# Kernel optimization log

Measured on AMD Instinct MI355X. Metric: run time of the kernel, lower is better.

Reference implementation:

```python
import jax, jax.numpy as jnp
import numpy as np

B, C, H, W = 16, 512, 32, 32
HID = 4 * C


def setup_inputs() -> dict:
    key = jax.random.key(0)
    k_x, k_w1, k_w2 = jax.random.split(key, 3)
    x = jax.random.normal(k_x, (B, C, H, W), dtype=jnp.float32)
    # 1x1 conv weights stored as [out, in] matrices (kernel_size=1)
    w1 = jax.random.normal(k_w1, (HID, C), dtype=jnp.float32) * (1.0 / np.sqrt(C))
    b1 = jnp.zeros((HID,), dtype=jnp.float32)
    w2 = jax.random.normal(k_w2, (C, HID), dtype=jnp.float32) * (1.0 / np.sqrt(HID))
    b2 = jnp.zeros((C,), dtype=jnp.float32)
    return {"x": x, "w1": w1, "b1": b1, "w2": w2, "b2": b2}


def reference(x, w1, b1, w2, b2):
    Bd, Cd, Hd, Wd = x.shape
    scale = Cd ** (-0.5)
    xf = x.reshape(Bd, Cd, Hd * Wd)          # [B, C, N]
    q = jnp.swapaxes(xf, -1, -2)              # [B, N, C]
    # full spatial self-attention: scores [B, N, N]
    attn = jax.nn.softmax(jnp.einsum('bnc,bcm->bnm', q, xf) * scale, axis=-1)
    out = jnp.einsum('bnm,bmc->bnc', attn, q)  # [B, N, C]
    # 1x1-conv FFN applied per spatial position
    h = jax.nn.relu(jnp.einsum('bnc,dc->bnd', out, w1) + b1)   # [B, N, 4C]
    y = jnp.einsum('bnd,cd->bnc', h, w2) + b2                  # [B, N, C]
    y = jnp.swapaxes(y, -1, -2).reshape(Bd, Cd, Hd, Wd)
    return y + x
```

## Files before the change

kernel.cpp:

```cpp
#include <hip/hip_runtime.h>

#define BATCH 16
#define CH    512
#define NSP   1024
#define HIDD  2048

typedef __bf16 bf16x8 __attribute__((ext_vector_type(8)));
typedef float floatx4 __attribute__((ext_vector_type(4)));

__device__ __forceinline__ float bf2f(unsigned short u) {
    union { unsigned int i; float f; } v; v.i = ((unsigned int)u) << 16; return v.f;
}
__device__ __forceinline__ unsigned short f2bf(float f) {
    union { float f; unsigned int i; } v; v.f = f;
    unsigned int i = v.i;
    return (unsigned short)((i + 0x7FFFu + ((i >> 16) & 1u)) >> 16);
}

__device__ __forceinline__ void gload16(const void* g, void* l) {
    __builtin_amdgcn_global_load_lds(
        (__attribute__((address_space(1))) unsigned int*)(g),
        (__attribute__((address_space(3))) unsigned int*)(l),
        16, 0, 0);
}

template<int EPI, int MAP>
__global__ __launch_bounds__(256, 4)
void gemm_bt(const unsigned short* __restrict__ A,
             const unsigned short* __restrict__ Bm,
             void* __restrict__ Cout,
             int Nn, int K,
             long sAb, long sBb, long sCb,
             const float* __restrict__ bias, float scale,
             const float* __restrict__ resid)
{
    __shared__ unsigned short sA[2][128 * 32];
    __shared__ unsigned short sB[2][128 * 32];

    const int tid  = threadIdx.x;
    const int lane = tid & 63;
    const int w    = tid >> 6;
    const int quad = lane >> 4;
    const int l15  = lane & 15;
    const int mw   = (w >> 1) * 64;
    const int nw   = (w & 1) * 64;

    const int F = blockIdx.x;
    int m0, n0, b;
    if constexpr (MAP == 0) {
        const int xcd = F & 7, s = F >> 3;
        b = xcd + ((s >> 6) << 3);
        const int j = s & 63; m0 = (j >> 3) << 7; n0 = (j & 7) << 7;
    } else if constexpr (MAP == 1) {
        const int xcd = F & 7, s = F >> 3;
        b = xcd + ((s >> 5) << 3);
        const int j = s & 31; m0 = (j >> 2) << 7; n0 = (j & 3) << 7;
    } else if constexpr (MAP == 2) {
        const int xcd = F & 7, s = F >> 3;
        b = 0; m0 = ((xcd << 4) + (s >> 4)) << 7; n0 = (s & 15) << 7;
    } else {
        const int xcd = F & 7, s = F >> 3;
        b = 0; m0 = (s & 3) << 7; n0 = ((xcd << 4) + (s >> 2)) << 7;
    }

    A  += (size_t)b * sAb;
    Bm += (size_t)b * sBb;

    const int srow = lane >> 2;
    const int sg   = (lane & 3) ^ ((lane >> 3) & 3);
    const unsigned short* pA = A  + (size_t)(m0 + w * 32 + srow) * K + sg * 8;
    const unsigned short* pB = Bm + (size_t)(n0 + w * 32 + srow) * K + sg * 8;
    const size_t rowskip16 = (size_t)16 * K;
    const int woff = w * 1024;

    floatx4 acc[4][4];
#pragma unroll
    for (int i = 0; i < 4; i++)
#pragma unroll
        for (int j = 0; j < 4; j++) acc[i][j] = (floatx4){0.f, 0.f, 0.f, 0.f};

    const int rslot = ((l15 >> 1) & 3);

    const int nIter = K >> 5;

    {
        unsigned short* dA = &sA[0][0] + woff;
        unsigned short* dB = &sB[0][0] + woff;
        gload16(pA,             dA);
        gload16(pA + rowskip16, dA + 512);
        gload16(pB,             dB);
        gload16(pB + rowskip16, dB + 512);
    }

    for (int it = 0; it < nIter; ++it) {
        __syncthreads();

        if (it + 1 < nIter) {
            const int koff = (it + 1) << 5;
            unsigned short* dA = &sA[(it + 1) & 1][0] + woff;
            unsigned short* dB = &sB[(it + 1) & 1][0] + woff;
            gload16(pA + koff,             dA);
            gload16(pA + koff + rowskip16, dA + 512);
            gload16(pB + koff,             dB);
            gload16(pB + koff + rowskip16, dB + 512);
        }

        const unsigned short* bufA = &sA[it & 1][0];
        const unsigned short* bufB = &sB[it & 1][0];
        bf16x8 af[4], bfr[4];
#pragma unroll
        for (int mi = 0; mi < 4; mi++)
            af[mi] = *(const bf16x8*)(bufA + (mw + mi * 16 + l15) * 32
                                      + (quad ^ rslot) * 8);
#pragma unroll
        for (int ni = 0; ni < 4; ni++)
            bfr[ni] = *(const bf16x8*)(bufB + (nw + ni * 16 + l15) * 32
                                       + (quad ^ rslot) * 8);
#pragma unroll
        for (int mi = 0; mi < 4; mi++)
#pragma unroll
            for (int ni = 0; ni < 4; ni++)
                acc[mi][ni] = __builtin_amdgcn_mfma_f32_16x16x32_bf16(
                    af[mi], bfr[ni], acc[mi][ni], 0, 0, 0);
    }

    if constexpr (EPI == 4) {
        float* Of = (float*)Cout;
#pragma unroll
        for (int ni = 0; ni < 4; ni++) {
            const int j  = n0 + nw + ni * 16 + l15;
            const int bb = j >> 10, ns = j & 1023;
            const size_t cbase = (size_t)bb * CH * NSP + ns;
#pragma unroll
            for (int mi = 0; mi < 4; mi++) {
                const int ibase = m0 + mw + mi * 16 + quad * 4;
#pragma unroll
                for (int r = 0; r < 4; r++) {
                    const int c = ibase + r;
                    const size_t a = cbase + (size_t)c * NSP;
                    Of[a] = acc[mi][ni][r] + bias[c] + resid[a];
                }
            }
        }
    } else {
        unsigned short* Cb = (unsigned short*)Cout + (size_t)b * sCb;
#pragma unroll
        for (int ni = 0; ni < 4; ni++) {
            const int n = n0 + nw + ni * 16 + l15;
            float bv = 0.f;
            if constexpr (EPI == 2) bv = bias[n];
#pragma unroll
            for (int mi = 0; mi < 4; mi++) {
                const int mbase = m0 + mw + mi * 16 + quad * 4;
#pragma unroll
                for (int r = 0; r < 4; r++) {
                    float v = acc[mi][ni][r];
                    if constexpr (EPI == 0) v *= scale;
                    if constexpr (EPI == 2) v = fmaxf(v + bv, 0.f);
                    Cb[(size_t)(mbase + r) * Nn + n] = f2bf(v);
                }
            }
        }
    }
}

__global__ __launch_bounds__(256)
void pack_x_kernel(const float* __restrict__ x,
                   unsigned short* __restrict__ Xbf,
                   unsigned short* __restrict__ XT)
{
    __shared__ float tile[32][33];
    const int tx = threadIdx.x, ty = threadIdx.y;
    const int n0 = blockIdx.x * 32, c0 = blockIdx.y * 32, b = blockIdx.z;
    const size_t base = (size_t)b * CH * NSP;
#pragma unroll
    for (int i = ty; i < 32; i += 8) {
        float v = x[base + (size_t)(c0 + i) * NSP + n0 + tx];
        tile[i][tx] = v;
        Xbf[base + (size_t)(c0 + i) * NSP + n0 + tx] = f2bf(v);
    }
    __syncthreads();
    const size_t tbase = (size_t)b * NSP * CH;
#pragma unroll
    for (int i = ty; i < 32; i += 8)
        XT[tbase + (size_t)(n0 + i) * CH + c0 + tx] = f2bf(tile[tx][i]);
}

__global__ __launch_bounds__(256)
void cast_bf16_kernel(const float* __restrict__ src,
                      unsigned short* __restrict__ dst, int n)
{
    int i = blockIdx.x * 256 + threadIdx.x;
    if (i < n) dst[i] = f2bf(src[i]);
}

__global__ __launch_bounds__(256)
void softmax_kernel(unsigned short* __restrict__ S)
{
    const int row = blockIdx.x;
    unsigned short* p = S + (size_t)row * NSP;
    const int t = threadIdx.x;

    ushort4 u = ((const ushort4*)p)[t];
    float v0 = bf2f(u.x), v1 = bf2f(u.y), v2 = bf2f(u.z), v3 = bf2f(u.w);

    float m = fmaxf(fmaxf(v0, v1), fmaxf(v2, v3));
#pragma unroll
    for (int off = 32; off > 0; off >>= 1) m = fmaxf(m, __shfl_xor(m, off));
    __shared__ float redmax[4], redsum[4];
    const int wid = t >> 6;
    if ((t & 63) == 0) redmax[wid] = m;
    __syncthreads();
    m = fmaxf(fmaxf(redmax[0], redmax[1]), fmaxf(redmax[2], redmax[3]));

    v0 = __expf(v0 - m); v1 = __expf(v1 - m);
    v2 = __expf(v2 - m); v3 = __expf(v3 - m);
    float s = v0 + v1 + v2 + v3;
#pragma unroll
    for (int off = 32; off > 0; off >>= 1) s += __shfl_xor(s, off);
    if ((t & 63) == 0) redsum[wid] = s;
    __syncthreads();
    s = redsum[0] + redsum[1] + redsum[2] + redsum[3];

    const float inv = 1.0f / s;
    ushort4 o;
    o.x = f2bf(v0 * inv); o.y = f2bf(v1 * inv);
    o.z = f2bf(v2 * inv); o.w = f2bf(v3 * inv);
    ((ushort4*)p)[t] = o;
}

extern "C" void kernel_launch(void* const* d_in, const int* in_sizes, int n_in,
                              void* d_out, int out_size, void* d_ws, size_t ws_size,
                              hipStream_t stream)
{
    const float* x  = (const float*)d_in[0];
    const float* w1 = (const float*)d_in[1];
    const float* b1 = (const float*)d_in[2];
    const float* w2 = (const float*)d_in[3];
    const float* b2 = (const float*)d_in[4];
    float* out = (float*)d_out;

    char* ws = (char*)d_ws;
    unsigned short* Xbf = (unsigned short*)ws; ws += (size_t)BATCH * CH * NSP * 2;
    unsigned short* XT  = (unsigned short*)ws; ws += (size_t)BATCH * NSP * CH * 2;
    unsigned short* W1b = (unsigned short*)ws; ws += (size_t)HIDD * CH * 2;
    unsigned short* W2b = (unsigned short*)ws; ws += (size_t)CH * HIDD * 2;
    unsigned short* P   = (unsigned short*)ws; ws += (size_t)BATCH * NSP * NSP * 2;
    unsigned short* O   = (unsigned short*)ws; ws += (size_t)BATCH * NSP * CH * 2;
    unsigned short* Hb  = (unsigned short*)ws; ws += (size_t)BATCH * NSP * HIDD * 2;

    const dim3 blk(256);

    pack_x_kernel<<<dim3(NSP / 32, CH / 32, BATCH), dim3(32, 8), 0, stream>>>(x, Xbf, XT);
    cast_bf16_kernel<<<dim3((HIDD * CH) / 256), blk, 0, stream>>>(w1, W1b, HIDD * CH);
    cast_bf16_kernel<<<dim3((CH * HIDD) / 256), blk, 0, stream>>>(w2, W2b, CH * HIDD);

    gemm_bt<0, 0><<<dim3(1024), blk, 0, stream>>>(
        XT, XT, P, NSP, CH,
        (long)NSP * CH, (long)NSP * CH, (long)NSP * NSP, nullptr,
        0.04419417382415922f, nullptr);

    softmax_kernel<<<dim3(BATCH * NSP), blk, 0, stream>>>(P);

    gemm_bt<1, 1><<<dim3(512), blk, 0, stream>>>(
        P, Xbf, O, CH, NSP,
        (long)NSP * NSP, (long)CH * NSP, (long)NSP * CH, nullptr, 1.f, nullptr);

    gemm_bt<2, 2><<<dim3(2048), blk, 0, stream>>>(
        O, W1b, Hb, HIDD, CH, 0, 0, 0, b1, 1.f, nullptr);

    gemm_bt<4, 3><<<dim3(512), blk, 0, stream>>>(
        W2b, Hb, out, BATCH * NSP, HIDD, 0, 0, 0, b2, 1.f, x);
}
```

Measured before the change: 282.2 us.

## Load B fragments directly to registers and triple-buffer A in LDS

The GEMM main loop stops staging the B operand through shared memory. Each wave now loads its B MFMA fragments straight from global memory into a pair of ping-pong registers, prefetched one step ahead. The A operand moves to a three-slot LDS ring with two-deep prefetch, and the explicit vmcnt wait plus barrier replaces __syncthreads. The aim is to cut LDS traffic and barrier stalls, at the cost of more VGPRs (occupancy hint lowered from 4 to 3) and uncoalesced direct global reads of B. The MAP==2 block mapping also drops its XCD-aware swizzle in favour of a plain linear order.

```diff
diff --git a/kernel.cpp b/kernel.cpp
--- a/kernel.cpp
+++ b/kernel.cpp
@@ -23,9 +23,10 @@
         (__attribute__((address_space(3))) unsigned int*)(l),
         16, 0, 0);
 }
+#define MEMFENCE asm volatile("" ::: "memory")
 
 template<int EPI, int MAP>
-__global__ __launch_bounds__(256, 4)
+__global__ __launch_bounds__(256, 3)
 void gemm_bt(const unsigned short* __restrict__ A,
              const unsigned short* __restrict__ Bm,
              void* __restrict__ Cout,
@@ -34,8 +35,7 @@
              const float* __restrict__ bias, float scale,
              const float* __restrict__ resid)
 {
-    __shared__ unsigned short sA[2][128 * 32];
-    __shared__ unsigned short sB[2][128 * 32];
+    __shared__ unsigned short sA[3][128 * 32];
 
     const int tid  = threadIdx.x;
     const int lane = tid & 63;
@@ -56,8 +56,7 @@
         b = xcd + ((s >> 5) << 3);
         const int j = s & 31; m0 = (j >> 2) << 7; n0 = (j & 3) << 7;
     } else if constexpr (MAP == 2) {
-        const int xcd = F & 7, s = F >> 3;
-        b = 0; m0 = ((xcd << 4) + (s >> 4)) << 7; n0 = (s & 15) << 7;
+        b = 0; m0 = (F >> 4) << 7; n0 = (F & 15) << 7;
     } else {
         const int xcd = F & 7, s = F >> 3;
         b = 0; m0 = (s & 3) << 7; n0 = ((xcd << 4) + (s >> 2)) << 7;
@@ -68,10 +67,13 @@
 
     const int srow = lane >> 2;
     const int sg   = (lane & 3) ^ ((lane >> 3) & 3);
-    const unsigned short* pA = A  + (size_t)(m0 + w * 32 + srow) * K + sg * 8;
-    const unsigned short* pB = Bm + (size_t)(n0 + w * 32 + srow) * K + sg * 8;
+    const unsigned short* pA = A + (size_t)(m0 + w * 32 + srow) * K + sg * 8;
     const size_t rowskip16 = (size_t)16 * K;
     const int woff = w * 1024;
+    const int rslot = ((l15 >> 1) & 3);
+
+    const unsigned short* pBf = Bm + (size_t)(n0 + nw + l15) * K + quad * 8;
+    const size_t bstride = (size_t)16 * K;
 
     floatx4 acc[4][4];
 #pragma unroll
@@ -79,49 +81,58 @@
 #pragma unroll
         for (int j = 0; j < 4; j++) acc[i][j] = (floatx4){0.f, 0.f, 0.f, 0.f};
 
-    const int rslot = ((l15 >> 1) & 3);
-
     const int nIter = K >> 5;
+    const int kLast = K - 32;
+
+    bf16x8 bP[4], bQ[4];
 
     {
-        unsigned short* dA = &sA[0][0] + woff;
-        unsigned short* dB = &sB[0][0] + woff;
-        gload16(pA,             dA);
-        gload16(pA + rowskip16, dA + 512);
-        gload16(pB,             dB);
-        gload16(pB + rowskip16, dB + 512);
-    }
-
-    for (int it = 0; it < nIter; ++it) {
-        __syncthreads();
-
-        if (it + 1 < nIter) {
-            const int koff = (it + 1) << 5;
-            unsigned short* dA = &sA[(it + 1) & 1][0] + woff;
-            unsigned short* dB = &sB[(it + 1) & 1][0] + woff;
-            gload16(pA + koff,             dA);
-            gload16(pA + koff + rowskip16, dA + 512);
-            gload16(pB + koff,             dB);
-            gload16(pB + koff + rowskip16, dB + 512);
-        }
-
-        const unsigned short* bufA = &sA[it & 1][0];
-        const unsigned short* bufB = &sB[it & 1][0];
-        bf16x8 af[4], bfr[4];
+        unsigned short* d0 = &sA[0][0] + woff;
+        unsigned short* d1 = &sA[1][0] + woff;
+        gload16(pA,                 d0);
+        gload16(pA + rowskip16,     d0 + 512);
+        gload16(pA + 32,            d1);
+        gload16(pA + 32 + rowskip16, d1 + 512);
+        MEMFENCE;
+#pragma unroll
+        for (int ni = 0; ni < 4; ni++)
+            bP[ni] = *(const bf16x8*)(pBf + ni * bstride);
+        MEMFENCE;
+    }
+
+    auto body = [&](int it, bf16x8* bcur, bf16x8* bnext) {
+        asm volatile("s_waitcnt vmcnt(6)\n\ts_barrier" ::: "memory");
+
+        int r = it; while (r >= 3) r -= 3;
+        int rs = r + 2; if (rs >= 3) rs -= 3;
+        const int kst = (it + 2) * 32 <= kLast ? (it + 2) * 32 : kLast;
+        unsigned short* dS = &sA[0][0] + rs * 4096 + woff;
+        gload16(pA + kst,             dS);
+        gload16(pA + kst + rowskip16, dS + 512);
+        MEMFENCE;
+        const int kb = (it + 1) * 32 <= kLast ? (it + 1) * 32 : kLast;
+#pragma unroll
+        for (int ni = 0; ni < 4; ni++)
+            bnext[ni] = *(const bf16x8*)(pBf + ni * bstride + kb);
+        MEMFENCE;
+
+        const unsigned short* bufR = &sA[0][0] + r * 4096;
+        bf16x8 af[4];
 #pragma unroll
         for (int mi = 0; mi < 4; mi++)
-            af[mi] = *(const bf16x8*)(bufA + (mw + mi * 16 + l15) * 32
+            af[mi] = *(const bf16x8*)(bufR + (mw + mi * 16 + l15) * 32
                                       + (quad ^ rslot) * 8);
-#pragma unroll
-        for (int ni = 0; ni < 4; ni++)
-            bfr[ni] = *(const bf16x8*)(bufB + (nw + ni * 16 + l15) * 32
-                                       + (quad ^ rslot) * 8);
 #pragma unroll
         for (int mi = 0; mi < 4; mi++)
 #pragma unroll
             for (int ni = 0; ni < 4; ni++)
                 acc[mi][ni] = __builtin_amdgcn_mfma_f32_16x16x32_bf16(
-                    af[mi], bfr[ni], acc[mi][ni], 0, 0, 0);
+                    af[mi], bcur[ni], acc[mi][ni], 0, 0, 0);
+    };
+
+    for (int it = 0; it < nIter; it += 2) {
+        body(it,     bP, bQ);
+        body(it + 1, bQ, bP);
     }
 
     if constexpr (EPI == 4) {
@@ -135,10 +146,10 @@
             for (int mi = 0; mi < 4; mi++) {
                 const int ibase = m0 + mw + mi * 16 + quad * 4;
 #pragma unroll
-                for (int r = 0; r < 4; r++) {
-                    const int c = ibase + r;
+                for (int r2 = 0; r2 < 4; r2++) {
+                    const int c = ibase + r2;
                     const size_t a = cbase + (size_t)c * NSP;
-                    Of[a] = acc[mi][ni][r] + bias[c] + resid[a];
+                    Of[a] = acc[mi][ni][r2] + bias[c] + resid[a];
                 }
             }
         }
@@ -153,11 +164,11 @@
             for (int mi = 0; mi < 4; mi++) {
                 const int mbase = m0 + mw + mi * 16 + quad * 4;
 #pragma unroll
-                for (int r = 0; r < 4; r++) {
-                    float v = acc[mi][ni][r];
+                for (int r2 = 0; r2 < 4; r2++) {
+                    float v = acc[mi][ni][r2];
                     if constexpr (EPI == 0) v *= scale;
                     if constexpr (EPI == 2) v = fmaxf(v + bv, 0.f);
-                    Cb[(size_t)(mbase + r) * Nn + n] = f2bf(v);
+                    Cb[(size_t)(mbase + r2) * Nn + n] = f2bf(v);
                 }
             }
         }
```

Measured after the change: 360.7 us. +27.8%, slower.

## Triple-buffer LDS tiles with two-stage prefetch and partial vmcnt waits

Applied to the files above, without the earlier changes.

Moves the GEMM mainloop from double to triple buffering in shared memory. Two K-tiles are now prefetched ahead, and each iteration waits only for the oldest outstanding global-to-LDS loads (vmcnt(4)) before the barrier instead of a full sync, so more load latency can overlap with MFMA work. On the last iterations the prefetch is clamped to reissue the final tile rather than branching. Launch bounds drop to 3 blocks per CU to make room for the larger LDS footprint, and the MAP==2 block-to-tile mapping drops its XCD swizzle in favour of a plain linear order, which may change L2 locality. Possible risks are an LDS race, since the buffer written by each prefetch was read in the previous iteration and is protected only by the next barrier, and lower occupancy.

```diff
diff --git a/kernel.cpp b/kernel.cpp
--- a/kernel.cpp
+++ b/kernel.cpp
@@ -23,9 +23,10 @@
         (__attribute__((address_space(3))) unsigned int*)(l),
         16, 0, 0);
 }
+#define MEMFENCE asm volatile("" ::: "memory")
 
 template<int EPI, int MAP>
-__global__ __launch_bounds__(256, 4)
+__global__ __launch_bounds__(256, 3)
 void gemm_bt(const unsigned short* __restrict__ A,
              const unsigned short* __restrict__ Bm,
              void* __restrict__ Cout,
@@ -34,8 +35,8 @@
              const float* __restrict__ bias, float scale,
              const float* __restrict__ resid)
 {
-    __shared__ unsigned short sA[2][128 * 32];
-    __shared__ unsigned short sB[2][128 * 32];
+    __shared__ unsigned short sA[3][128 * 32];
+    __shared__ unsigned short sB[3][128 * 32];
 
     const int tid  = threadIdx.x;
     const int lane = tid & 63;
@@ -56,8 +57,7 @@
         b = xcd + ((s >> 5) << 3);
         const int j = s & 31; m0 = (j >> 2) << 7; n0 = (j & 3) << 7;
     } else if constexpr (MAP == 2) {
-        const int xcd = F & 7, s = F >> 3;
-        b = 0; m0 = ((xcd << 4) + (s >> 4)) << 7; n0 = (s & 15) << 7;
+        b = 0; m0 = (F >> 4) << 7; n0 = (F & 15) << 7;
     } else {
         const int xcd = F & 7, s = F >> 3;
         b = 0; m0 = (s & 3) << 7; n0 = ((xcd << 4) + (s >> 2)) << 7;
@@ -72,6 +72,7 @@
     const unsigned short* pB = Bm + (size_t)(n0 + w * 32 + srow) * K + sg * 8;
     const size_t rowskip16 = (size_t)16 * K;
     const int woff = w * 1024;
+    const int rslot = ((l15 >> 1) & 3);
 
     floatx4 acc[4][4];
 #pragma unroll
@@ -79,34 +80,40 @@
 #pragma unroll
         for (int j = 0; j < 4; j++) acc[i][j] = (floatx4){0.f, 0.f, 0.f, 0.f};
 
-    const int rslot = ((l15 >> 1) & 3);
-
     const int nIter = K >> 5;
+    const int kLast = K - 32;
 
     {
-        unsigned short* dA = &sA[0][0] + woff;
-        unsigned short* dB = &sB[0][0] + woff;
-        gload16(pA,             dA);
-        gload16(pA + rowskip16, dA + 512);
-        gload16(pB,             dB);
-        gload16(pB + rowskip16, dB + 512);
-    }
-
+        unsigned short* dA0 = &sA[0][0] + woff;
+        unsigned short* dB0 = &sB[0][0] + woff;
+        gload16(pA,                  dA0);
+        gload16(pA + rowskip16,      dA0 + 512);
+        gload16(pB,                  dB0);
+        gload16(pB + rowskip16,      dB0 + 512);
+        unsigned short* dA1 = &sA[1][0] + woff;
+        unsigned short* dB1 = &sB[1][0] + woff;
+        gload16(pA + 32,             dA1);
+        gload16(pA + 32 + rowskip16, dA1 + 512);
+        gload16(pB + 32,             dB1);
+        gload16(pB + 32 + rowskip16, dB1 + 512);
+        MEMFENCE;
+    }
+
+    int bcur = 0, bpf = 2;
     for (int it = 0; it < nIter; ++it) {
-        __syncthreads();
-
-        if (it + 1 < nIter) {
-            const int koff = (it + 1) << 5;
-            unsigned short* dA = &sA[(it + 1) & 1][0] + woff;
-            unsigned short* dB = &sB[(it + 1) & 1][0] + woff;
-            gload16(pA + koff,             dA);
-            gload16(pA + koff + rowskip16, dA + 512);
-            gload16(pB + koff,             dB);
-            gload16(pB + koff + rowskip16, dB + 512);
-        }
-
-        const unsigned short* bufA = &sA[it & 1][0];
-        const unsigned short* bufB = &sB[it & 1][0];
+        asm volatile("s_waitcnt vmcnt(4)\n\ts_barrier" ::: "memory");
+
+        const int kpf = (it + 2) * 32 <= kLast ? (it + 2) * 32 : kLast;
+        unsigned short* dA = &sA[0][0] + bpf * 4096 + woff;
+        unsigned short* dB = &sB[0][0] + bpf * 4096 + woff;
+        gload16(pA + kpf,             dA);
+        gload16(pA + kpf + rowskip16, dA + 512);
+        gload16(pB + kpf,             dB);
+        gload16(pB + kpf + rowskip16, dB + 512);
+        MEMFENCE;
+
+        const unsigned short* bufA = &sA[0][0] + bcur * 4096;
+        const unsigned short* bufB = &sB[0][0] + bcur * 4096;
         bf16x8 af[4], bfr[4];
 #pragma unroll
         for (int mi = 0; mi < 4; mi++)
@@ -122,7 +129,11 @@
             for (int ni = 0; ni < 4; ni++)
                 acc[mi][ni] = __builtin_amdgcn_mfma_f32_16x16x32_bf16(
                     af[mi], bfr[ni], acc[mi][ni], 0, 0, 0);
-    }
+
+        bcur = bcur == 2 ? 0 : bcur + 1;
+        bpf  = bpf  == 2 ? 0 : bpf  + 1;
+    }
+    asm volatile("s_waitcnt vmcnt(0)" ::: "memory");
 
     if constexpr (EPI == 4) {
         float* Of = (float*)Cout;
```

New measurement: 278.6 us. No clear change (-1.3%).
